# Optimization experiments

Hardware: AMD Instinct MI355X
Metric: run time of the kernel (lower is better)

## Reference

```python
import jax, jax.numpy as jnp
import numpy as np


def setup_inputs() -> dict:
    key = jax.random.key(0)
    k1, k2, k3 = jax.random.split(key, 3)
    n, seq_len, hidden = 100000, 4, 128
    n_edges = 1600000
    semantics = jax.random.normal(k1, (n, seq_len, hidden), dtype=jnp.float32)
    attention_masks = jnp.ones((n, seq_len, hidden), dtype=jnp.float32)
    W = jax.random.normal(k2, (hidden, hidden), dtype=jnp.float32) * (1.0 / np.sqrt(hidden))
    edge_index = jax.random.randint(k3, (n_edges, 2), 0, n, dtype=jnp.int64)
    return {"semantics": semantics, "attention_masks": attention_masks, "W": W, "edge_index": edge_index}


def reference(semantics, attention_masks, W, edge_index):
    # semantics: (n, seq_len, hidden); only token 0 is used.
    # edge_index: (E, 2) = adj.nonzero(); col 0 = source (gather), col 1 = target (scatter).
    n = semantics.shape[0]
    h = semantics[:, 0] @ W                         # (n, hidden)
    src = h[edge_index[:, 0]]                       # (E, hidden) gather
    tgt = edge_index[:, 1]
    sums = jax.ops.segment_sum(src, tgt, num_segments=n)            # (n, hidden)
    cnt = jax.ops.segment_sum(jnp.ones((edge_index.shape[0],), dtype=h.dtype), tgt, num_segments=n)
    h_mean = sums / jnp.maximum(cnt, 1.0)[:, None]  # scatter_mean; untouched rows stay 0
    return jax.nn.gelu(h_mean, approximate=False)
```

## Files before the change

### kernel.cpp

```cpp
#include <hip/hip_runtime.h>
#include <math.h>


#define SLOT 64

__global__ __launch_bounds__(256) void fill_csr(const int* __restrict__ edges,
        int* __restrict__ cnt, int* __restrict__ csr, int n_edges) {
    int t = blockIdx.x * blockDim.x + threadIdx.x;
    int base = t * 4;
    if (base + 3 < n_edges) {
        int4 a = ((const int4*)edges)[t * 2];
        int4 b = ((const int4*)edges)[t * 2 + 1];
        int src[4] = {a.x, a.z, b.x, b.z};
        int tgt[4] = {a.y, a.w, b.y, b.w};
        int pos[4];
        #pragma unroll
        for (int i = 0; i < 4; i++) pos[i] = atomicAdd(&cnt[tgt[i]], 1);
        #pragma unroll
        for (int i = 0; i < 4; i++)
            if (pos[i] < SLOT) csr[(size_t)tgt[i] * SLOT + pos[i]] = src[i];
    } else if (base < n_edges) {
        for (int e = base; e < n_edges; e++) {
            int2 p = ((const int2*)edges)[e];
            int pos = atomicAdd(&cnt[p.y], 1);
            if (pos < SLOT) csr[(size_t)p.y * SLOT + pos] = p.x;
        }
    }
}

__global__ __launch_bounds__(256) void gather_mean(
        const float* __restrict__ sem, const int* __restrict__ cnt,
        const int* __restrict__ csr, float* __restrict__ mean, int n) {
    int gid  = blockIdx.x * blockDim.x + threadIdx.x;
    int node = gid >> 6;
    int lane = gid & 63;
    if (node >= n) return;

    int deg = cnt[node];
    int m   = min(deg, SLOT);
    int sv  = (lane < m) ? csr[(size_t)node * SLOT + lane] : 0;

    const int half = lane >> 5;
    const int q    = lane & 31;

    float4 acc = make_float4(0.f, 0.f, 0.f, 0.f);

    int j = 0;
    for (; j + 16 <= m; j += 16) {
        int s[8];
        #pragma unroll
        for (int u = 0; u < 8; u++) s[u] = __shfl(sv, j + 2 * u + half);
        float4 v[8];
        #pragma unroll
        for (int u = 0; u < 8; u++)
            v[u] = ((const float4*)(sem + (size_t)s[u] * 512))[q];
        #pragma unroll
        for (int u = 0; u < 8; u++) {
            acc.x += v[u].x; acc.y += v[u].y; acc.z += v[u].z; acc.w += v[u].w;
        }
    }
    for (; j + 2 <= m; j += 2) {
        int s = __shfl(sv, j + half);
        float4 v = ((const float4*)(sem + (size_t)s * 512))[q];
        acc.x += v.x; acc.y += v.y; acc.z += v.z; acc.w += v.w;
    }
    if (j < m) {
        int s = __shfl(sv, j);
        if (half == 0) {
            float4 v = ((const float4*)(sem + (size_t)s * 512))[q];
            acc.x += v.x; acc.y += v.y; acc.z += v.z; acc.w += v.w;
        }
    }

    float4 oth;
    oth.x = __shfl(acc.x, (lane + 32) & 63);
    oth.y = __shfl(acc.y, (lane + 32) & 63);
    oth.z = __shfl(acc.z, (lane + 32) & 63);
    oth.w = __shfl(acc.w, (lane + 32) & 63);

    if (half == 0) {
        float inv = 1.0f / fmaxf((float)deg, 1.0f);
        float4 t = make_float4((acc.x + oth.x) * inv, (acc.y + oth.y) * inv,
                               (acc.z + oth.z) * inv, (acc.w + oth.w) * inv);
        ((float4*)(mean + (size_t)node * 128))[q] = t;
    }
}

__device__ __forceinline__ float gelu_exact(float x) {
    return 0.5f * x * (1.0f + erff(x * 0.70710678118654752f));
}
__device__ __forceinline__ void fma4(float m, const float4 w, float4& a) {
    a.x = fmaf(m, w.x, a.x); a.y = fmaf(m, w.y, a.y);
    a.z = fmaf(m, w.z, a.z); a.w = fmaf(m, w.w, a.w);
}

__global__ __launch_bounds__(256) void finalize_kernel(
        const float* __restrict__ W, float* __restrict__ io, int n) {
    __shared__ float ml[64 * 128];

    const int cg = threadIdx.x & 31;
    const int rb = threadIdx.x >> 5;
    const int rowsPerIter = 64 * gridDim.x;

    for (int row0 = blockIdx.x * 64; row0 < n; row0 += rowsPerIter) {
        __syncthreads();
        #pragma unroll
        for (int p = 0; p < 8; p++) {
            int fid = threadIdx.x + 256 * p;
            int rr = fid >> 5, k4 = fid & 31;
            int row = row0 + rr;
            if (row < n)
                ((float4*)ml)[fid] = ((const float4*)(io + (size_t)row * 128))[k4];
        }
        __syncthreads();

        float4 acc[8];
        #pragma unroll
        for (int i = 0; i < 8; i++) acc[i] = make_float4(0.f, 0.f, 0.f, 0.f);

        const float* mbase = ml + rb * 8 * 128;

        for (int kc = 0; kc < 16; kc++) {
            float4 wreg[8];
            #pragma unroll
            for (int u = 0; u < 8; u++)
                wreg[u] = ((const float4*)(W + (size_t)(kc * 8 + u) * 128))[cg];
            #pragma unroll
            for (int rr = 0; rr < 8; rr++) {
                const float4* mrow = (const float4*)(mbase + rr * 128);
                float4 mlo = mrow[kc * 2], mhi = mrow[kc * 2 + 1];
                fma4(mlo.x, wreg[0], acc[rr]);
                fma4(mlo.y, wreg[1], acc[rr]);
                fma4(mlo.z, wreg[2], acc[rr]);
                fma4(mlo.w, wreg[3], acc[rr]);
                fma4(mhi.x, wreg[4], acc[rr]);
                fma4(mhi.y, wreg[5], acc[rr]);
                fma4(mhi.z, wreg[6], acc[rr]);
                fma4(mhi.w, wreg[7], acc[rr]);
            }
        }

        #pragma unroll
        for (int rr = 0; rr < 8; rr++) {
            int row = row0 + rb * 8 + rr;
            if (row < n) {
                float4 g = make_float4(gelu_exact(acc[rr].x), gelu_exact(acc[rr].y),
                                       gelu_exact(acc[rr].z), gelu_exact(acc[rr].w));
                ((float4*)(io + (size_t)row * 128))[cg] = g;
            }
        }
    }
}

extern "C" void kernel_launch(void* const* d_in, const int* in_sizes, int n_in,
                              void* d_out, int out_size, void* d_ws, size_t ws_size,
                              hipStream_t stream) {
    const float* sem   = (const float*)d_in[0];
    const float* W     = (const float*)d_in[2];
    const int*   edges = (const int*)d_in[3];

    const int n       = in_sizes[0] / (4 * 128);
    const int n_edges = in_sizes[3] / 2;

    char* p = (char*)d_ws;
    int* cnt = (int*)p;   p += (((size_t)n * 4) + 15) & ~(size_t)15;
    int* csr = (int*)p;

    hipMemsetAsync(cnt, 0, (size_t)n * 4, stream);

    const int T = 256;
    const int fthreads = (n_edges + 3) / 4;
    fill_csr   <<<(fthreads + T - 1) / T, T, 0, stream>>>(edges, cnt, csr, n_edges);

    const int gblocks = (int)(((long long)n * 64 + T - 1) / T);
    gather_mean<<<gblocks, T, 0, stream>>>(sem, cnt, csr, (float*)d_out, n);

    finalize_kernel<<<1024, T, 0, stream>>>(W, (float*)d_out, n);
}
```

Baseline: 623.8 us.

## Project rows before gather and co-schedule CSR fill with matmul in one kernel

Reorders the computation so the 128x128 projection runs first on token 0 of each row, writing a compact h buffer. The gather then reads 128-float rows of h instead of strided rows of the semantics tensor, and GELU is applied in the same pass. The CSR build and the matmul now share one launch: blocks are interleaved by index (one matmul block per six fill blocks), so the atomic-bound fill overlaps compute-bound work. In exchange it needs an extra n×128 workspace buffer and one extra write and read of h. The fill also loses its four-edges-per-thread batching.

```diff
diff --git a/kernel.cpp b/kernel.cpp
--- a/kernel.cpp
+++ b/kernel.cpp
@@ -3,88 +3,6 @@
 
 
 #define SLOT 64
-
-__global__ __launch_bounds__(256) void fill_csr(const int* __restrict__ edges,
-        int* __restrict__ cnt, int* __restrict__ csr, int n_edges) {
-    int t = blockIdx.x * blockDim.x + threadIdx.x;
-    int base = t * 4;
-    if (base + 3 < n_edges) {
-        int4 a = ((const int4*)edges)[t * 2];
-        int4 b = ((const int4*)edges)[t * 2 + 1];
-        int src[4] = {a.x, a.z, b.x, b.z};
-        int tgt[4] = {a.y, a.w, b.y, b.w};
-        int pos[4];
-        #pragma unroll
-        for (int i = 0; i < 4; i++) pos[i] = atomicAdd(&cnt[tgt[i]], 1);
-        #pragma unroll
-        for (int i = 0; i < 4; i++)
-            if (pos[i] < SLOT) csr[(size_t)tgt[i] * SLOT + pos[i]] = src[i];
-    } else if (base < n_edges) {
-        for (int e = base; e < n_edges; e++) {
-            int2 p = ((const int2*)edges)[e];
-            int pos = atomicAdd(&cnt[p.y], 1);
-            if (pos < SLOT) csr[(size_t)p.y * SLOT + pos] = p.x;
-        }
-    }
-}
-
-__global__ __launch_bounds__(256) void gather_mean(
-        const float* __restrict__ sem, const int* __restrict__ cnt,
-        const int* __restrict__ csr, float* __restrict__ mean, int n) {
-    int gid  = blockIdx.x * blockDim.x + threadIdx.x;
-    int node = gid >> 6;
-    int lane = gid & 63;
-    if (node >= n) return;
-
-    int deg = cnt[node];
-    int m   = min(deg, SLOT);
-    int sv  = (lane < m) ? csr[(size_t)node * SLOT + lane] : 0;
-
-    const int half = lane >> 5;
-    const int q    = lane & 31;
-
-    float4 acc = make_float4(0.f, 0.f, 0.f, 0.f);
-
-    int j = 0;
-    for (; j + 16 <= m; j += 16) {
-        int s[8];
-        #pragma unroll
-        for (int u = 0; u < 8; u++) s[u] = __shfl(sv, j + 2 * u + half);
-        float4 v[8];
-        #pragma unroll
-        for (int u = 0; u < 8; u++)
-            v[u] = ((const float4*)(sem + (size_t)s[u] * 512))[q];
-        #pragma unroll
-        for (int u = 0; u < 8; u++) {
-            acc.x += v[u].x; acc.y += v[u].y; acc.z += v[u].z; acc.w += v[u].w;
-        }
-    }
-    for (; j + 2 <= m; j += 2) {
-        int s = __shfl(sv, j + half);
-        float4 v = ((const float4*)(sem + (size_t)s * 512))[q];
-        acc.x += v.x; acc.y += v.y; acc.z += v.z; acc.w += v.w;
-    }
-    if (j < m) {
-        int s = __shfl(sv, j);
-        if (half == 0) {
-            float4 v = ((const float4*)(sem + (size_t)s * 512))[q];
-            acc.x += v.x; acc.y += v.y; acc.z += v.z; acc.w += v.w;
-        }
-    }
-
-    float4 oth;
-    oth.x = __shfl(acc.x, (lane + 32) & 63);
-    oth.y = __shfl(acc.y, (lane + 32) & 63);
-    oth.z = __shfl(acc.z, (lane + 32) & 63);
-    oth.w = __shfl(acc.w, (lane + 32) & 63);
-
-    if (half == 0) {
-        float inv = 1.0f / fmaxf((float)deg, 1.0f);
-        float4 t = make_float4((acc.x + oth.x) * inv, (acc.y + oth.y) * inv,
-                               (acc.z + oth.z) * inv, (acc.w + oth.w) * inv);
-        ((float4*)(mean + (size_t)node * 128))[q] = t;
-    }
-}
 
 __device__ __forceinline__ float gelu_exact(float x) {
     return 0.5f * x * (1.0f + erff(x * 0.70710678118654752f));
@@ -94,15 +12,31 @@
     a.z = fmaf(m, w.z, a.z); a.w = fmaf(m, w.w, a.w);
 }
 
-__global__ __launch_bounds__(256) void finalize_kernel(
-        const float* __restrict__ W, float* __restrict__ io, int n) {
+__global__ __launch_bounds__(256) void fill_and_matmul(
+        const int* __restrict__ edges, int* __restrict__ cnt,
+        int* __restrict__ csr, int n_edges,
+        const float* __restrict__ sem, const float* __restrict__ W,
+        float* __restrict__ h, int n, int mm_blocks) {
     __shared__ float ml[64 * 128];
 
+    int bid = blockIdx.x;
+    if (bid % 7 != 0) {
+        int fb = bid - bid / 7 - 1;
+        int e  = fb * 256 + (int)threadIdx.x;
+        if (e < n_edges) {
+            int2 p = ((const int2*)edges)[e];
+            int pos = atomicAdd(&cnt[p.y], 1);
+            if (pos < SLOT) csr[(size_t)p.y * SLOT + pos] = p.x;
+        }
+        return;
+    }
+
+    int mb = bid / 7;
     const int cg = threadIdx.x & 31;
     const int rb = threadIdx.x >> 5;
-    const int rowsPerIter = 64 * gridDim.x;
+    const int rowsPerIter = 64 * mm_blocks;
 
-    for (int row0 = blockIdx.x * 64; row0 < n; row0 += rowsPerIter) {
+    for (int row0 = mb * 64; row0 < n; row0 += rowsPerIter) {
         __syncthreads();
         #pragma unroll
         for (int p = 0; p < 8; p++) {
@@ -110,7 +44,7 @@
             int rr = fid >> 5, k4 = fid & 31;
             int row = row0 + rr;
             if (row < n)
-                ((float4*)ml)[fid] = ((const float4*)(io + (size_t)row * 128))[k4];
+                ((float4*)ml)[fid] = ((const float4*)(sem + (size_t)row * 512))[k4];
         }
         __syncthreads();
 
@@ -143,12 +77,69 @@
         #pragma unroll
         for (int rr = 0; rr < 8; rr++) {
             int row = row0 + rb * 8 + rr;
-            if (row < n) {
-                float4 g = make_float4(gelu_exact(acc[rr].x), gelu_exact(acc[rr].y),
-                                       gelu_exact(acc[rr].z), gelu_exact(acc[rr].w));
-                ((float4*)(io + (size_t)row * 128))[cg] = g;
-            }
+            if (row < n)
+                ((float4*)(h + (size_t)row * 128))[cg] = acc[rr];
         }
+    }
+}
+
+__global__ __launch_bounds__(256) void gather_gelu(
+        const float* __restrict__ h, const int* __restrict__ cnt,
+        const int* __restrict__ csr, float* __restrict__ out, int n) {
+    int gid  = blockIdx.x * blockDim.x + threadIdx.x;
+    int node = gid >> 6;
+    int lane = gid & 63;
+    if (node >= n) return;
+
+    int deg = cnt[node];
+    int m   = min(deg, SLOT);
+    int sv  = (lane < m) ? csr[(size_t)node * SLOT + lane] : 0;
+
+    const int half = lane >> 5;
+    const int q    = lane & 31;
+
+    float4 acc = make_float4(0.f, 0.f, 0.f, 0.f);
+
+    int j = 0;
+    for (; j + 16 <= m; j += 16) {
+        int s[8];
+        #pragma unroll
+        for (int u = 0; u < 8; u++) s[u] = __shfl(sv, j + 2 * u + half);
+        float4 v[8];
+        #pragma unroll
+        for (int u = 0; u < 8; u++)
+            v[u] = ((const float4*)(h + (size_t)s[u] * 128))[q];
+        #pragma unroll
+        for (int u = 0; u < 8; u++) {
+            acc.x += v[u].x; acc.y += v[u].y; acc.z += v[u].z; acc.w += v[u].w;
+        }
+    }
+    for (; j + 2 <= m; j += 2) {
+        int s = __shfl(sv, j + half);
+        float4 v = ((const float4*)(h + (size_t)s * 128))[q];
+        acc.x += v.x; acc.y += v.y; acc.z += v.z; acc.w += v.w;
+    }
+    if (j < m) {
+        int s = __shfl(sv, j);
+        if (half == 0) {
+            float4 v = ((const float4*)(h + (size_t)s * 128))[q];
+            acc.x += v.x; acc.y += v.y; acc.z += v.z; acc.w += v.w;
+        }
+    }
+
+    float4 oth;
+    oth.x = __shfl(acc.x, (lane + 32) & 63);
+    oth.y = __shfl(acc.y, (lane + 32) & 63);
+    oth.z = __shfl(acc.z, (lane + 32) & 63);
+    oth.w = __shfl(acc.w, (lane + 32) & 63);
+
+    if (half == 0) {
+        float inv = 1.0f / fmaxf((float)deg, 1.0f);
+        float4 t = make_float4(gelu_exact((acc.x + oth.x) * inv),
+                               gelu_exact((acc.y + oth.y) * inv),
+                               gelu_exact((acc.z + oth.z) * inv),
+                               gelu_exact((acc.w + oth.w) * inv));
+        ((float4*)(out + (size_t)node * 128))[q] = t;
     }
 }
 
@@ -162,18 +153,22 @@
     const int n       = in_sizes[0] / (4 * 128);
     const int n_edges = in_sizes[3] / 2;
 
+    auto align16 = [](size_t x) { return (x + 15) & ~(size_t)15; };
     char* p = (char*)d_ws;
-    int* cnt = (int*)p;   p += (((size_t)n * 4) + 15) & ~(size_t)15;
-    int* csr = (int*)p;
+    int*   cnt = (int*)p;    p += align16((size_t)n * 4);
+    int*   csr = (int*)p;    p += align16((size_t)n * SLOT * 4);
+    float* h   = (float*)p;
 
     hipMemsetAsync(cnt, 0, (size_t)n * 4, stream);
 
-    const int T = 256;
-    const int fthreads = (n_edges + 3) / 4;
-    fill_csr   <<<(fthreads + T - 1) / T, T, 0, stream>>>(edges, cnt, csr, n_edges);
+    const int T  = 256;
+    const int FB = (n_edges + T - 1) / T;
+    const int total = (FB * 7 + 5) / 6;
+    const int MB    = total - FB;
+
+    fill_and_matmul<<<total, T, 0, stream>>>(edges, cnt, csr, n_edges,
+                                             sem, W, h, n, MB);
 
     const int gblocks = (int)(((long long)n * 64 + T - 1) / T);
-    gather_mean<<<gblocks, T, 0, stream>>>(sem, cnt, csr, (float*)d_out, n);
-
-    finalize_kernel<<<1024, T, 0, stream>>>(W, (float*)d_out, n);
+    gather_gelu<<<gblocks, T, 0, stream>>>(h, cnt, csr, (float*)d_out, n);
 }
```

Measured after the change: 553.9 us. -11.2%, faster.
